# Kernel optimization log

Hardware: AMD Instinct MI355X
Metric: run time of the kernel (lower is better)

The kernel has to match this reference:

```python
import jax, jax.numpy as jnp
import numpy as np

GLM_HIDDEN = 256
K = 3
REL_NUM = K + 1
NUM_BASES = 2
BATCH = 8
SLEN = 2048


def setup_inputs() -> dict:
    key = jax.random.key(0)
    k1, k2, k3, k4, k5 = jax.random.split(key, 5)
    D = GLM_HIDDEN
    x = jax.random.normal(k1, (BATCH, SLEN, D), dtype=jnp.float32)
    # RGCNConv basis decomposition params: W_r = sum_b comp[r,b] * basis[b]
    scale = 1.0 / np.sqrt(D)
    basis = jax.random.normal(k2, (NUM_BASES, D, D), dtype=jnp.float32) * scale
    comp = jax.random.normal(k3, (REL_NUM, NUM_BASES), dtype=jnp.float32)
    root = jax.random.normal(k4, (D, D), dtype=jnp.float32) * scale
    bias = jax.random.normal(k5, (D,), dtype=jnp.float32) * 0.01
    return {"x": x, "comp": comp, "basis": basis, "root": root, "bias": bias}


def reference(x, comp, basis, root, bias):
    B, S, D = x.shape
    R = comp.shape[0]
    Kthr = R - 1
    idx = jnp.arange(S)
    # edge (source s -> target t) has relation min(|t+1 - s|, K); full S x S edge set
    rel = jnp.minimum(jnp.abs((idx[None, :] + 1) - idx[:, None]), Kthr)  # [S(source), S(target)]
    masks = (rel[None, :, :] == jnp.arange(R)[:, None, None]).astype(x.dtype)  # [R,S,T]
    deg = masks.sum(axis=1)  # [R,T] in-degree per relation (PyG aggr='mean')
    inv_deg = jnp.where(deg > 0, 1.0 / deg, 0.0)
    A = masks * inv_deg[:, None, :]  # normalized adjacency per relation [R,S,T]
    # basis-decomposed relation weights
    W = jnp.einsum('rb,bio->rio', comp, basis)  # [R,D,D]
    # aggregate then transform: out[b,t] = sum_r (mean_{s in N_r(t)} x[b,s]) @ W_r
    agg = jnp.einsum('rst,bsi->brti', A, x)  # [B,R,S,D]
    out = jnp.einsum('brti,rio->bto', agg, W)
    out = out + jnp.einsum('bsi,io->bso', x, root) + bias
    return out
```

## Files before the change

### kernel.cpp

```cpp
#include <hip/hip_runtime.h>

#define D 256
#define S 2048
#define B 8
#define DSQ (D * D)
#define INV3 (1.0f / 2043.0f)

typedef __bf16 bf16x8 __attribute__((ext_vector_type(8)));
typedef float f32x4 __attribute__((ext_vector_type(4)));

__device__ __forceinline__ unsigned short f2bf(float f) {
    union { float f; unsigned int u; } v; v.f = f;
    unsigned int u = v.u;
    u += 0x7fffu + ((u >> 16) & 1u);
    return (unsigned short)(u >> 16);
}

__device__ __forceinline__ void gl2lds16(const void* g, void* l) {
    __builtin_amdgcn_global_load_lds(
        (const __attribute__((address_space(1))) void*)g,
        (__attribute__((address_space(3))) void*)l, 16, 0, 0);
}

__global__ __launch_bounds__(256) void k_prep(const float* __restrict__ x,
                                              const float* __restrict__ comp,
                                              const float* __restrict__ basis,
                                              const float* __restrict__ root,
                                              unsigned short* __restrict__ xh,
                                              float* __restrict__ part,
                                              unsigned short* __restrict__ Cbs) {
    int blk = blockIdx.x;
    int tid = threadIdx.x;
    int b = blk >> 6, chunk = blk & 63;
    __shared__ float ps[4][D];
    int rg = tid >> 6;
    int c4 = (tid & 63) << 2;
    int row0 = chunk * 32 + rg * 8;
    const float4* xb = (const float4*)(x + ((size_t)b * S + row0) * D + c4);
    ushort4* dst = (ushort4*)(xh + ((size_t)(1 + b * S + row0)) * D + c4);
    float4 s = {0.f, 0.f, 0.f, 0.f};
    #pragma unroll
    for (int i = 0; i < 8; ++i) {
        float4 v = xb[(size_t)i * 64];
        ushort4 o;
        o.x = f2bf(v.x); o.y = f2bf(v.y); o.z = f2bf(v.z); o.w = f2bf(v.w);
        dst[(size_t)i * 64] = o;
        s.x += v.x; s.y += v.y; s.z += v.z; s.w += v.w;
    }
    *(float4*)&ps[rg][c4] = s;

    if (blk < 160) {
        int step = blk >> 2, q = blk & 3;
        int ji = step >> 3, kc = step & 7;
        int n = tid;
        float a0 = (ji == 2) ? 1.f : 0.f;
        float a1 = (ji == 1 || ji == 3) ? 0.5f : 0.f;
        float a2 = (ji == 0 || ji == 4) ? 0.5f : 0.f;
        float ar = (ji == 1) ? 1.f : 0.f;
        float cb0 = a0 * comp[0] + a1 * comp[2] + a2 * comp[4] - INV3 * comp[6];
        float cb1 = a0 * comp[1] + a1 * comp[3] + a2 * comp[5] - INV3 * comp[7];
        unsigned short buf[8];
        #pragma unroll
        for (int kk = 0; kk < 8; ++kk) {
            int i = kc * 32 + q * 8 + kk;
            buf[kk] = f2bf(cb0 * basis[i * D + n] + cb1 * basis[DSQ + i * D + n]
                           + ar * root[i * D + n]);
        }
        *(uint4*)(Cbs + ((size_t)step * 256 + n) * 32 + q * 8) = *(uint4*)buf;
    }
    __syncthreads();
    if (tid < 64)
        *(float4*)&part[(size_t)blk * D + tid * 4] =
            *(float4*)&ps[0][tid * 4] + *(float4*)&ps[1][tid * 4] +
            *(float4*)&ps[2][tid * 4] + *(float4*)&ps[3][tid * 4];
}

__global__ __launch_bounds__(256) void k_weights(
        const float* __restrict__ basis, const float* __restrict__ comp,
        const float* __restrict__ root, const float* __restrict__ bias,
        const float* __restrict__ part, const float* __restrict__ x,
        float* __restrict__ Tb, float* __restrict__ out) {
    int blk = blockIdx.x;
    int tid = threadIdx.x;

    if (blk < 8) {
        int b = blk;
        __shared__ float tot[D];
        float t = 0.f;
        #pragma unroll 8
        for (int c = 0; c < 64; ++c) t += part[(size_t)(b * 64 + c) * D + tid];
        tot[tid] = t;
        __syncthreads();
        int o = tid;
        float c30 = comp[6], c31 = comp[7];
        float acc = 0.f;
        #pragma unroll 4
        for (int k = 0; k < D; ++k)
            acc += tot[k] * (c30 * basis[k * D + o] + c31 * basis[DSQ + k * D + o]);
        Tb[b * D + o] = bias[o] + acc * INV3;
    } else {
        int r = blk - 8;
        const int tl[4] = {0, S - 3, S - 2, S - 1};
        int t = tl[r & 3], b = r >> 2;
        __shared__ float z0[D], z1[D], xr[D];
        const float* xb = x + (size_t)b * S * D;
        int i = tid;
        float tot = 0.f;
        #pragma unroll 8
        for (int c = 0; c < 64; ++c) tot += part[(size_t)(b * 64 + c) * D + i];
        float x_t = xb[(size_t)t * D + i];
        float v0 = (t + 1 < S) ? xb[(size_t)(t + 1) * D + i] : 0.f;
        float d1 = 1.f + ((t + 2 < S) ? 1.f : 0.f);
        float v1 = (x_t + ((t + 2 < S) ? xb[(size_t)(t + 2) * D + i] : 0.f)) / d1;
        float s2 = ((t - 1 >= 0) ? xb[(size_t)(t - 1) * D + i] : 0.f)
                 + ((t + 3 < S) ? xb[(size_t)(t + 3) * D + i] : 0.f);
        int d2i = ((t - 1 >= 0) ? 1 : 0) + ((t + 3 < S) ? 1 : 0);
        float v2 = d2i ? s2 / (float)d2i : 0.f;
        float wsum = 0.f;
        for (int s = t - 1; s <= t + 3; ++s)
            if (s >= 0 && s < S) wsum += xb[(size_t)s * D + i];
        int d3i = ((t - 1 > 0) ? (t - 1) : 0) + ((S - 4 - t > 0) ? (S - 4 - t) : 0);
        float v3 = d3i ? (tot - wsum) / (float)d3i : 0.f;
        z0[i] = comp[0] * v0 + comp[2] * v1 + comp[4] * v2 + comp[6] * v3;
        z1[i] = comp[1] * v0 + comp[3] * v1 + comp[5] * v2 + comp[7] * v3;
        xr[i] = x_t;
        __syncthreads();
        int o = tid;
        float acc = 0.f;
        #pragma unroll 8
        for (int k = 0; k < D; ++k)
            acc += z0[k] * basis[k * D + o] + z1[k] * basis[DSQ + k * D + o]
                 + xr[k] * root[k * D + o];
        out[(((size_t)b * S + t) << 8) + o] = acc + bias[o];
    }
}

__global__ __launch_bounds__(256) void k_bulk(
        const unsigned short* __restrict__ xh,
        const unsigned short* __restrict__ Cbs,
        const float* __restrict__ Tb,
        float* __restrict__ out) {
    __shared__ __align__(16) unsigned short xs[68 * 256];
    const int tid  = threadIdx.x;
    const int lane = tid & 63;
    const int w    = tid >> 6;
    const int blk  = blockIdx.x;
    const int nblk = blk & 1;
    const int mblk = blk >> 1;
    const int b    = mblk >> 5;
    const int t0   = (mblk & 31) << 6;
    const size_t rowbase = (size_t)b * S + t0;

    #pragma unroll
    for (int q = 0; q < 8; ++q) {
        int F = (q * 256 + tid) * 16;
        int r = F >> 9;
        int c16 = (F >> 4) & 31;
        int gc = (c16 & 24) | ((c16 ^ r) & 7);
        gl2lds16((const char*)xh + ((rowbase + r) << 9) + (gc << 4), (char*)xs + F);
    }
    if (tid < 128) {
        int F = (2048 + tid) * 16;
        int r = F >> 9;
        int c16 = (F >> 4) & 31;
        int gc = (c16 & 24) | ((c16 ^ r) & 7);
        gl2lds16((const char*)xh + ((rowbase + r) << 9) + (gc << 4), (char*)xs + F);
    }
    __syncthreads();

    const int rlo = lane & 15, q4 = lane >> 4;
    const int nstrip = nblk * 128 + w * 32;

    #define BFRAG(st, nt) (*(const bf16x8*)(Cbs + \
        (((size_t)(st) * 256 + nstrip + (nt) * 16 + rlo) << 5) + (q4 << 3)))
    #define AFRAG(st, mt) (*(const bf16x8*)((const char*)xs + \
        ((((mt) * 16 + rlo + ((st) >> 3))) << 9) + \
        (((((st) & 7) * 4 + q4) & 24 | ((((st) & 7) * 4 + q4) ^ \
          ((mt) * 16 + rlo + ((st) >> 3))) & 7) << 4)))

    f32x4 acc[4][2] = {};
    bf16x8 bb[4][2];
    bf16x8 aa[2][4];
    #pragma unroll
    for (int nt = 0; nt < 2; ++nt) {
        bb[0][nt] = BFRAG(0, nt); bb[1][nt] = BFRAG(1, nt); bb[2][nt] = BFRAG(2, nt);
    }
    #pragma unroll
    for (int mt = 0; mt < 4; ++mt) aa[0][mt] = AFRAG(0, mt);

    #pragma unroll
    for (int step = 0; step < 40; ++step) {
        const int pfB = (step + 3 < 40) ? step + 3 : 39;
        #pragma unroll
        for (int nt = 0; nt < 2; ++nt) bb[(step + 3) & 3][nt] = BFRAG(pfB, nt);
        const int pfA = (step + 1 < 40) ? step + 1 : 39;
        #pragma unroll
        for (int mt = 0; mt < 4; ++mt) aa[(step + 1) & 1][mt] = AFRAG(pfA, mt);

        #pragma unroll
        for (int mt = 0; mt < 4; ++mt)
            #pragma unroll
            for (int nt = 0; nt < 2; ++nt)
                acc[mt][nt] = __builtin_amdgcn_mfma_f32_16x16x32_bf16(
                    aa[step & 1][mt], bb[step & 3][nt], acc[mt][nt], 0, 0, 0);
    }
    #undef BFRAG
    #undef AFRAG

    const int col = lane & 15, rq = (lane >> 4) << 2;
    #pragma unroll
    for (int nt = 0; nt < 2; ++nt) {
        int n = nstrip + nt * 16 + col;
        float tb = Tb[b * D + n];
        #pragma unroll
        for (int mt = 0; mt < 4; ++mt) {
            #pragma unroll
            for (int i = 0; i < 4; ++i) {
                int t = t0 + mt * 16 + rq + i;
                if (t >= 1 && t <= S - 4)
                    out[(((size_t)b * S + t) << 8) + n] = acc[mt][nt][i] + tb;
            }
        }
    }
}


extern "C" void kernel_launch(void* const* d_in, const int* in_sizes, int n_in,
                              void* d_out, int out_size, void* d_ws, size_t ws_size,
                              hipStream_t stream) {
    const float* x     = (const float*)d_in[0];
    const float* comp  = (const float*)d_in[1];
    const float* basis = (const float*)d_in[2];
    const float* root  = (const float*)d_in[3];
    const float* bias  = (const float*)d_in[4];
    float* out = (float*)d_out;

    char* ws = (char*)d_ws;
    float* part         = (float*)(ws);
    float* Tb           = (float*)(ws + 524288);
    unsigned short* Cbs = (unsigned short*)(ws + 532480);
    unsigned short* xh  = (unsigned short*)(ws + 1187840);

    k_prep   <<<512, 256, 0, stream>>>(x, comp, basis, root, xh, part, Cbs);
    k_weights<<<40,  256, 0, stream>>>(basis, comp, root, bias, part, x, Tb, out);
    k_bulk   <<<512, 256, 0, stream>>>(xh, Cbs, Tb, out);
}
```

Baseline: 117.0 us.

## Fuse weights kernel into bulk GEMM with atomic flag handoff for bias term

Merges the small k_weights kernel into the bulk MFMA kernel. The first 8 blocks compute the per-batch bias vector Tb and the next 32 blocks compute the boundary rows, both overlapped with the async LDS load of x. A device-scope release/acquire flag makes every block wait for Tb before its epilogue. This drops one kernel launch and the serial gap between launches, at the cost of a spin-wait and extra work on a few blocks, which could stall if blocks are not co-resident.

```diff
diff --git a/kernel.cpp b/kernel.cpp
--- a/kernel.cpp
+++ b/kernel.cpp
@@ -28,7 +28,8 @@
                                               const float* __restrict__ root,
                                               unsigned short* __restrict__ xh,
                                               float* __restrict__ part,
-                                              unsigned short* __restrict__ Cbs) {
+                                              unsigned short* __restrict__ Cbs,
+                                              unsigned int* __restrict__ flag) {
     int blk = blockIdx.x;
     int tid = threadIdx.x;
     int b = blk >> 6, chunk = blk & 63;
@@ -68,6 +69,7 @@
         }
         *(uint4*)(Cbs + ((size_t)step * 256 + n) * 32 + q * 8) = *(uint4*)buf;
     }
+    if (blk == 0 && tid == 0) *flag = 0u;
     __syncthreads();
     if (tid < 64)
         *(float4*)&part[(size_t)blk * D + tid * 4] =
@@ -75,17 +77,63 @@
             *(float4*)&ps[2][tid * 4] + *(float4*)&ps[3][tid * 4];
 }
 
-__global__ __launch_bounds__(256) void k_weights(
+__global__ __launch_bounds__(256, 2) void k_bulk2(
+        const unsigned short* __restrict__ xh,
+        const unsigned short* __restrict__ Cbs,
         const float* __restrict__ basis, const float* __restrict__ comp,
         const float* __restrict__ root, const float* __restrict__ bias,
         const float* __restrict__ part, const float* __restrict__ x,
-        float* __restrict__ Tb, float* __restrict__ out) {
-    int blk = blockIdx.x;
-    int tid = threadIdx.x;
+        float* __restrict__ Tb, unsigned int* __restrict__ flag,
+        float* __restrict__ out) {
+    __shared__ __align__(16) unsigned short xs[68 * 256];
+    __shared__ __align__(16) float aux[4 * D];
+    const int tid  = threadIdx.x;
+    const int lane = tid & 63;
+    const int w    = tid >> 6;
+    const int blk  = blockIdx.x;
+    const int nblk = blk & 1;
+    const int mblk = blk >> 1;
+    const int bq   = mblk >> 5;
+    const int t0   = (mblk & 31) << 6;
+    const size_t rowbase = (size_t)bq * S + t0;
+
+    #pragma unroll
+    for (int q = 0; q < 8; ++q) {
+        int F = (q * 256 + tid) * 16;
+        int r = F >> 9;
+        int c16 = (F >> 4) & 31;
+        int gc = (c16 & 24) | ((c16 ^ r) & 7);
+        gl2lds16((const char*)xh + ((rowbase + r) << 9) + (gc << 4), (char*)xs + F);
+    }
+    if (tid < 128) {
+        int F = (2048 + tid) * 16;
+        int r = F >> 9;
+        int c16 = (F >> 4) & 31;
+        int gc = (c16 & 24) | ((c16 ^ r) & 7);
+        gl2lds16((const char*)xh + ((rowbase + r) << 9) + (gc << 4), (char*)xs + F);
+    }
+
+    const int rlo = lane & 15, q4 = lane >> 4;
+    const int nstrip = nblk * 128 + w * 32;
+
+    #define BFRAG(st, nt) (*(const bf16x8*)(Cbs + \
+        (((size_t)(st) * 256 + nstrip + (nt) * 16 + rlo) << 5) + (q4 << 3)))
+    #define AFRAG(st, mt) (*(const bf16x8*)((const char*)xs + \
+        ((((mt) * 16 + rlo + ((st) >> 3))) << 9) + \
+        (((((st) & 7) * 4 + q4) & 24 | ((((st) & 7) * 4 + q4) ^ \
+          ((mt) * 16 + rlo + ((st) >> 3))) & 7) << 4)))
+
+    f32x4 acc[4][2] = {};
+    bf16x8 bb[4][2];
+    bf16x8 aa[2][4];
+    #pragma unroll
+    for (int nt = 0; nt < 2; ++nt) {
+        bb[0][nt] = BFRAG(0, nt); bb[1][nt] = BFRAG(1, nt); bb[2][nt] = BFRAG(2, nt);
+    }
 
     if (blk < 8) {
-        int b = blk;
-        __shared__ float tot[D];
+        const int b = blk;
+        float* tot = aux;
         float t = 0.f;
         #pragma unroll 8
         for (int c = 0; c < 64; ++c) t += part[(size_t)(b * 64 + c) * D + tid];
@@ -93,98 +141,53 @@
         __syncthreads();
         int o = tid;
         float c30 = comp[6], c31 = comp[7];
-        float acc = 0.f;
+        float a2c = 0.f;
         #pragma unroll 4
         for (int k = 0; k < D; ++k)
-            acc += tot[k] * (c30 * basis[k * D + o] + c31 * basis[DSQ + k * D + o]);
-        Tb[b * D + o] = bias[o] + acc * INV3;
-    } else {
-        int r = blk - 8;
+            a2c += tot[k] * (c30 * basis[k * D + o] + c31 * basis[DSQ + k * D + o]);
+        Tb[b * D + o] = bias[o] + a2c * INV3;
+        __syncthreads();
+        if (tid == 0)
+            __hip_atomic_fetch_add(flag, 1u, __ATOMIC_RELEASE,
+                                   __HIP_MEMORY_SCOPE_AGENT);
+    } else if (blk < 40) {
+        const int r = blk - 8;
         const int tl[4] = {0, S - 3, S - 2, S - 1};
-        int t = tl[r & 3], b = r >> 2;
-        __shared__ float z0[D], z1[D], xr[D];
-        const float* xb = x + (size_t)b * S * D;
+        const int t = tl[r & 3], b2 = r >> 2;
+        float* z0 = aux; float* z1 = aux + D; float* xr = aux + 2 * D;
+        const float* xb2 = x + (size_t)b2 * S * D;
         int i = tid;
-        float tot = 0.f;
+        float tot2 = 0.f;
         #pragma unroll 8
-        for (int c = 0; c < 64; ++c) tot += part[(size_t)(b * 64 + c) * D + i];
-        float x_t = xb[(size_t)t * D + i];
-        float v0 = (t + 1 < S) ? xb[(size_t)(t + 1) * D + i] : 0.f;
+        for (int c = 0; c < 64; ++c) tot2 += part[(size_t)(b2 * 64 + c) * D + i];
+        float x_t = xb2[(size_t)t * D + i];
+        float v0 = (t + 1 < S) ? xb2[(size_t)(t + 1) * D + i] : 0.f;
         float d1 = 1.f + ((t + 2 < S) ? 1.f : 0.f);
-        float v1 = (x_t + ((t + 2 < S) ? xb[(size_t)(t + 2) * D + i] : 0.f)) / d1;
-        float s2 = ((t - 1 >= 0) ? xb[(size_t)(t - 1) * D + i] : 0.f)
-                 + ((t + 3 < S) ? xb[(size_t)(t + 3) * D + i] : 0.f);
+        float v1 = (x_t + ((t + 2 < S) ? xb2[(size_t)(t + 2) * D + i] : 0.f)) / d1;
+        float s2 = ((t - 1 >= 0) ? xb2[(size_t)(t - 1) * D + i] : 0.f)
+                 + ((t + 3 < S) ? xb2[(size_t)(t + 3) * D + i] : 0.f);
         int d2i = ((t - 1 >= 0) ? 1 : 0) + ((t + 3 < S) ? 1 : 0);
         float v2 = d2i ? s2 / (float)d2i : 0.f;
         float wsum = 0.f;
-        for (int s = t - 1; s <= t + 3; ++s)
-            if (s >= 0 && s < S) wsum += xb[(size_t)s * D + i];
+        for (int ss = t - 1; ss <= t + 3; ++ss)
+            if (ss >= 0 && ss < S) wsum += xb2[(size_t)ss * D + i];
         int d3i = ((t - 1 > 0) ? (t - 1) : 0) + ((S - 4 - t > 0) ? (S - 4 - t) : 0);
-        float v3 = d3i ? (tot - wsum) / (float)d3i : 0.f;
+        float v3 = d3i ? (tot2 - wsum) / (float)d3i : 0.f;
         z0[i] = comp[0] * v0 + comp[2] * v1 + comp[4] * v2 + comp[6] * v3;
         z1[i] = comp[1] * v0 + comp[3] * v1 + comp[5] * v2 + comp[7] * v3;
         xr[i] = x_t;
         __syncthreads();
         int o = tid;
-        float acc = 0.f;
+        float a2c = 0.f;
         #pragma unroll 8
         for (int k = 0; k < D; ++k)
-            acc += z0[k] * basis[k * D + o] + z1[k] * basis[DSQ + k * D + o]
+            a2c += z0[k] * basis[k * D + o] + z1[k] * basis[DSQ + k * D + o]
                  + xr[k] * root[k * D + o];
-        out[(((size_t)b * S + t) << 8) + o] = acc + bias[o];
-    }
-}
-
-__global__ __launch_bounds__(256) void k_bulk(
-        const unsigned short* __restrict__ xh,
-        const unsigned short* __restrict__ Cbs,
-        const float* __restrict__ Tb,
-        float* __restrict__ out) {
-    __shared__ __align__(16) unsigned short xs[68 * 256];
-    const int tid  = threadIdx.x;
-    const int lane = tid & 63;
-    const int w    = tid >> 6;
-    const int blk  = blockIdx.x;
-    const int nblk = blk & 1;
-    const int mblk = blk >> 1;
-    const int b    = mblk >> 5;
-    const int t0   = (mblk & 31) << 6;
-    const size_t rowbase = (size_t)b * S + t0;
-
-    #pragma unroll
-    for (int q = 0; q < 8; ++q) {
-        int F = (q * 256 + tid) * 16;
-        int r = F >> 9;
-        int c16 = (F >> 4) & 31;
-        int gc = (c16 & 24) | ((c16 ^ r) & 7);
-        gl2lds16((const char*)xh + ((rowbase + r) << 9) + (gc << 4), (char*)xs + F);
-    }
-    if (tid < 128) {
-        int F = (2048 + tid) * 16;
-        int r = F >> 9;
-        int c16 = (F >> 4) & 31;
-        int gc = (c16 & 24) | ((c16 ^ r) & 7);
-        gl2lds16((const char*)xh + ((rowbase + r) << 9) + (gc << 4), (char*)xs + F);
-    }
+        out[(((size_t)b2 * S + t) << 8) + o] = a2c + bias[o];
+    }
+
     __syncthreads();
 
-    const int rlo = lane & 15, q4 = lane >> 4;
-    const int nstrip = nblk * 128 + w * 32;
-
-    #define BFRAG(st, nt) (*(const bf16x8*)(Cbs + \
-        (((size_t)(st) * 256 + nstrip + (nt) * 16 + rlo) << 5) + (q4 << 3)))
-    #define AFRAG(st, mt) (*(const bf16x8*)((const char*)xs + \
-        ((((mt) * 16 + rlo + ((st) >> 3))) << 9) + \
-        (((((st) & 7) * 4 + q4) & 24 | ((((st) & 7) * 4 + q4) ^ \
-          ((mt) * 16 + rlo + ((st) >> 3))) & 7) << 4)))
-
-    f32x4 acc[4][2] = {};
-    bf16x8 bb[4][2];
-    bf16x8 aa[2][4];
-    #pragma unroll
-    for (int nt = 0; nt < 2; ++nt) {
-        bb[0][nt] = BFRAG(0, nt); bb[1][nt] = BFRAG(1, nt); bb[2][nt] = BFRAG(2, nt);
-    }
     #pragma unroll
     for (int mt = 0; mt < 4; ++mt) aa[0][mt] = AFRAG(0, mt);
 
@@ -207,18 +210,25 @@
     #undef BFRAG
     #undef AFRAG
 
+    if (tid == 0) {
+        while (__hip_atomic_load(flag, __ATOMIC_ACQUIRE,
+                                 __HIP_MEMORY_SCOPE_AGENT) < 8u)
+            __builtin_amdgcn_s_sleep(2);
+    }
+    __syncthreads();
+
     const int col = lane & 15, rq = (lane >> 4) << 2;
     #pragma unroll
     for (int nt = 0; nt < 2; ++nt) {
         int n = nstrip + nt * 16 + col;
-        float tb = Tb[b * D + n];
+        float tb = Tb[bq * D + n];
         #pragma unroll
         for (int mt = 0; mt < 4; ++mt) {
             #pragma unroll
             for (int i = 0; i < 4; ++i) {
                 int t = t0 + mt * 16 + rq + i;
                 if (t >= 1 && t <= S - 4)
-                    out[(((size_t)b * S + t) << 8) + n] = acc[mt][nt][i] + tb;
+                    out[(((size_t)bq * S + t) << 8) + n] = acc[mt][nt][i] + tb;
             }
         }
     }
@@ -240,8 +250,9 @@
     float* Tb           = (float*)(ws + 524288);
     unsigned short* Cbs = (unsigned short*)(ws + 532480);
     unsigned short* xh  = (unsigned short*)(ws + 1187840);
-
-    k_prep   <<<512, 256, 0, stream>>>(x, comp, basis, root, xh, part, Cbs);
-    k_weights<<<40,  256, 0, stream>>>(basis, comp, root, bias, part, x, Tb, out);
-    k_bulk   <<<512, 256, 0, stream>>>(xh, Cbs, Tb, out);
-}
+    unsigned int* flag  = (unsigned int*)(ws + 9580544);
+
+    k_prep <<<512, 256, 0, stream>>>(x, comp, basis, root, xh, part, Cbs, flag);
+    k_bulk2<<<512, 256, 0, stream>>>(xh, Cbs, basis, comp, root, bias, part, x,
+                                     Tb, flag, out);
+}
```

Result: slower. 182.7 us (+56.1%).
